# Optimization experiments

Hardware: AMD Instinct MI355X
Metric: run time of the kernel (lower is better)

## Reference

```python
import jax, jax.numpy as jnp
import numpy as np
from jax import lax

H = W = 8
N = H * W            # grid cells
D = 34               # token dim = 16 + 16 + 2
NH = 2               # attention heads
FF = 2048            # torch TransformerEncoderLayer default dim_feedforward
EPS = 1e-5


def setup_inputs():
    key = jax.random.key(0)
    ks = iter(jax.random.split(key, 64))
    rn = lambda shape, s=0.05: jax.random.normal(next(ks), shape, jnp.float32) * s
    inp = {"obs": jax.random.normal(next(ks), (2, H, W), jnp.float32), "action": 2}
    inp["conv1_w"] = rn((16, 2, 3, 3)); inp["conv1_b"] = rn((16,))
    inp["conv2_w"] = rn((16, 16, 3, 3)); inp["conv2_b"] = rn((16,))
    for l in range(2):
        p = f"l{l}_"
        inp[p + "in_w"] = rn((3 * D, D)); inp[p + "in_b"] = rn((3 * D,))
        inp[p + "out_w"] = rn((D, D)); inp[p + "out_b"] = rn((D,))
        inp[p + "ff1_w"] = rn((FF, D)); inp[p + "ff1_b"] = rn((FF,))
        inp[p + "ff2_w"] = rn((D, FF)); inp[p + "ff2_b"] = rn((D,))
        inp[p + "ln1_g"] = jnp.ones((D,)); inp[p + "ln1_b"] = jnp.zeros((D,))
        inp[p + "ln2_g"] = jnp.ones((D,)); inp[p + "ln2_b"] = jnp.zeros((D,))
    inp["act_w"] = rn((8, 4)); inp["act_b"] = rn((8,))
    inp["head_w"] = rn((16, D + 8)); inp["head_b"] = rn((16,))
    return inp


def _ln(x, g, b):
    m = x.mean(-1, keepdims=True)
    v = ((x - m) ** 2).mean(-1, keepdims=True)
    return (x - m) * lax.rsqrt(v + EPS) * g + b


def _mha(x, in_w, in_b, out_w, out_b):
    S = x.shape[0]
    hd = D // NH
    qkv = x @ in_w.T + in_b                          # [S, 3D]
    q, k, v = jnp.split(qkv, 3, axis=-1)
    q = q.reshape(S, NH, hd).transpose(1, 0, 2)      # [H, S, hd]
    k = k.reshape(S, NH, hd).transpose(1, 0, 2)
    v = v.reshape(S, NH, hd).transpose(1, 0, 2)
    attn = jax.nn.softmax(jnp.einsum('hsd,htd->hst', q, k) * (1.0 / float(np.sqrt(hd))), axis=-1)
    o = jnp.einsum('hst,htd->hsd', attn, v).transpose(1, 0, 2).reshape(S, D)
    return o @ out_w.T + out_b


def _layer(x, in_w, in_b, out_w, out_b, ff1_w, ff1_b, ff2_w, ff2_b, ln1_g, ln1_b, ln2_g, ln2_b):
    # torch default post-norm, relu activation, dropout off (eval)
    x = _ln(x + _mha(x, in_w, in_b, out_w, out_b), ln1_g, ln1_b)
    h = jax.nn.relu(x @ ff1_w.T + ff1_b) @ ff2_w.T + ff2_b
    return _ln(x + h, ln2_g, ln2_b)


def _forward(obs, conv1_w, conv1_b, conv2_w, conv2_b, layers, act_w, act_b, head_w, head_b, action):
    x = obs[None]                                    # [1, 2, H, W]
    dn = ('NCHW', 'OIHW', 'NCHW')
    x = jax.nn.relu(lax.conv_general_dilated(x, conv1_w, (1, 1), 'SAME', dimension_numbers=dn) + conv1_b[None, :, None, None])
    x = jax.nn.relu(lax.conv_general_dilated(x, conv2_w, (1, 1), 'SAME', dimension_numbers=dn) + conv2_b[None, :, None, None])
    cell = x.reshape(16, N).T                        # [N, 16]
    # vectorized pairwise relation tokens (replaces O(N^2) python loop)
    r = (jnp.arange(N) // W).astype(jnp.float32)
    c = (jnp.arange(N) % W).astype(jnp.float32)
    dx = (r[:, None] - r[None, :]) / ((H - 1) / 2.0)
    dy = (c[:, None] - c[None, :]) / ((W - 1) / 2.0)
    rel = jnp.stack([dx, dy], axis=-1)               # [N, N, 2]
    a = jnp.broadcast_to(cell[:, None, :], (N, N, 16))
    b = jnp.broadcast_to(cell[None, :, :], (N, N, 16))
    seq = jnp.concatenate([a, b, rel], axis=-1).reshape(N * N, D)
    for p in layers:
        seq = _layer(seq, *p)
    agent_idx = jnp.argmax(obs[0].reshape(-1))
    agent_tok = lax.dynamic_slice_in_dim(seq, agent_idx * N, N, 0)  # rows for agent cell
    hvec = agent_tok.mean(0)
    a_emb = jax.nn.relu(jax.nn.one_hot(action, 4, dtype=jnp.float32) @ act_w.T + act_b)
    return (jnp.concatenate([hvec, a_emb]) @ head_w.T + head_b)[None]


def reference(obs, action, conv1_w, conv1_b, conv2_w, conv2_b,
              l0_in_w, l0_in_b, l0_out_w, l0_out_b, l0_ff1_w, l0_ff1_b, l0_ff2_w, l0_ff2_b,
              l0_ln1_g, l0_ln1_b, l0_ln2_g, l0_ln2_b,
              l1_in_w, l1_in_b, l1_out_w, l1_out_b, l1_ff1_w, l1_ff1_b, l1_ff2_w, l1_ff2_b,
              l1_ln1_g, l1_ln1_b, l1_ln2_g, l1_ln2_b,
              act_w, act_b, head_w, head_b):
    layers = [
        (l0_in_w, l0_in_b, l0_out_w, l0_out_b, l0_ff1_w, l0_ff1_b, l0_ff2_w, l0_ff2_b, l0_ln1_g, l0_ln1_b, l0_ln2_g, l0_ln2_b),
        (l1_in_w, l1_in_b, l1_out_w, l1_out_b, l1_ff1_w, l1_ff1_b, l1_ff2_w, l1_ff2_b, l1_ln1_g, l1_ln1_b, l1_ln2_g, l1_ln2_b),
    ]
    return _forward(obs, conv1_w, conv1_b, conv2_w, conv2_b, layers, act_w, act_b, head_w, head_b, action)
```

## Files before the change

kernel.cpp:

```cpp
#include <hip/hip_runtime.h>
#include <math.h>

#define SEQ 4096
#define DIM 34
#define NHEAD 2
#define HD 17
#define FFDIM 2048
#define SC2 0.34990494f

#define EXP2F(x) __builtin_amdgcn_exp2f(x)
#define MFMA16(a, b, c) __builtin_amdgcn_mfma_f32_16x16x32_bf16(a, b, c, 0, 0, 0)

typedef unsigned short u16;
typedef __attribute__((ext_vector_type(8))) short bf16x8;
typedef __attribute__((ext_vector_type(4))) float f32x4;

__device__ inline u16 f2bf(float f) {
    uint32_t u = __builtin_bit_cast(uint32_t, f);
    u += 0x7fffu + ((u >> 16) & 1u);
    return (u16)(u >> 16);
}
__device__ inline uint32_t pack2(float a, float b) {
    uint32_t ua = __builtin_bit_cast(uint32_t, a);
    ua += 0x7fffu + ((ua >> 16) & 1u);
    uint32_t ub = __builtin_bit_cast(uint32_t, b);
    ub += 0x7fffu + ((ub >> 16) & 1u);
    return (ua >> 16) | (ub & 0xffff0000u);
}

#define W1B_ELEMS (FFDIM * 64)
#define W2B_ELEMS (48 * FFDIM)
#define NWCONV 448

__global__ __launch_bounds__(1024) void wm_pre(
    const float* __restrict__ obs,
    const float* __restrict__ c1w, const float* __restrict__ c1b,
    const float* __restrict__ c2w, const float* __restrict__ c2b,
    const float* __restrict__ in_w, const float* __restrict__ in_b,
    const float* __restrict__ w1a, const float* __restrict__ b1a, const float* __restrict__ w2a,
    const float* __restrict__ w1b, const float* __restrict__ b1b, const float* __restrict__ w2b,
    float* __restrict__ x, u16* __restrict__ Qb, u16* __restrict__ Kb,
    u16* __restrict__ Vc, u16* __restrict__ V16,
    u16* __restrict__ W1A, u16* __restrict__ W2A,
    u16* __restrict__ W1B, u16* __restrict__ W2B)
{
    const int tid = threadIdx.x;
    if (blockIdx.x < NWCONV) {
        int id = blockIdx.x * 1024 + tid;
        const int half = W1B_ELEMS + W2B_ELEMS;
        const float* w1 = w1a; const float* b1 = b1a; const float* w2 = w2a;
        u16* W1 = W1A; u16* W2 = W2A;
        if (id >= half) { id -= half; w1 = w1b; b1 = b1b; w2 = w2b; W1 = W1B; W2 = W2B; }
        if (id < W1B_ELEMS) {
            int n = id >> 6, c = id & 63;
            float v = (c < DIM) ? w1[n*DIM + c] : ((c == DIM) ? b1[n] : 0.f);
            W1[id] = f2bf(v);
        } else {
            int e = id - W1B_ELEMS;
            int n = e >> 11;
            float v = (n < DIM) ? w2[(n << 11) + (e & 2047)] : 0.f;
            W2[e] = f2bf(v);
        }
        return;
    }
    __shared__ float obsp[2][10][10];
    __shared__ float h1p[16][10][10];
    __shared__ float cs[64][17];
    const int sb = blockIdx.x - NWCONV;
    const int t0 = sb * 64;

    for (int e = tid; e < 200; e += 1024) ((float*)obsp)[e] = 0.f;
    for (int e = tid; e < 1600; e += 1024) ((float*)h1p)[e] = 0.f;
    __syncthreads();
    if (tid < 128) {
        int i = tid >> 6, n = tid & 63, y = n >> 3, xx = n & 7;
        obsp[i][y + 1][xx + 1] = obs[tid];
    }
    __syncthreads();
    {
        int o = tid >> 6, n = tid & 63, y = n >> 3, xx = n & 7;
        float a = c1b[o];
        #pragma unroll
        for (int i = 0; i < 2; ++i)
            #pragma unroll
            for (int ky = 0; ky < 3; ++ky)
                #pragma unroll
                for (int kx = 0; kx < 3; ++kx)
                    a = fmaf(obsp[i][y + ky][xx + kx], c1w[((o*2 + i)*3 + ky)*3 + kx], a);
        h1p[o][y + 1][xx + 1] = fmaxf(a, 0.f);
    }
    __syncthreads();
    {
        int o = tid >> 6, n = tid & 63, y = n >> 3, xx = n & 7;
        float a = c2b[o];
        #pragma unroll
        for (int i = 0; i < 16; ++i)
            #pragma unroll
            for (int ky = 0; ky < 3; ++ky)
                #pragma unroll
                for (int kx = 0; kx < 3; ++kx)
                    a = fmaf(h1p[i][y + ky][xx + kx], c2w[((o*16 + i)*3 + ky)*3 + kx], a);
        cs[n][o] = fmaxf(a, 0.f);
    }
    __syncthreads();
    for (int e = tid; e < 64 * DIM; e += 1024) {
        int tl = e / DIM, d = e % DIM;
        int t = t0 + tl, i = t >> 6, j = t & 63;
        float v;
        if (d < 16)       v = cs[i][d];
        else if (d < 32)  v = cs[j][d - 16];
        else if (d == 32) v = (float)((i >> 3) - (j >> 3)) * (1.0f / 3.5f);
        else              v = (float)((i & 7) - (j & 7)) * (1.0f / 3.5f);
        x[t0 * DIM + e] = v;
    }
    for (int ii = 0; ii < 11; ++ii) {
        int e = tid + ii * 1024;
        if (e >= 64 * 162) break;
        int t = t0 + (e & 63), slot = e >> 6;
        int i = t >> 6, j = t & 63;
        float dx = (float)((i >> 3) - (j >> 3)) * (1.0f / 3.5f);
        float dy = (float)((i & 7) - (j & 7)) * (1.0f / 3.5f);
        if (slot < 128) {
            int isK = slot >> 6, h2 = (slot >> 5) & 1, hs = slot & 31;
            float val = 0.f;
            if (hs < HD) {
                int row = isK*DIM + h2*HD + hs;
                const float* wr = in_w + row*DIM;
                float a = in_b[row];
                #pragma unroll
                for (int d = 0; d < 16; ++d) a = fmaf(cs[i][d], wr[d], a);
                #pragma unroll
                for (int d = 0; d < 16; ++d) a = fmaf(cs[j][d], wr[16 + d], a);
                a = fmaf(dx, wr[32], a);
                a = fmaf(dy, wr[33], a);
                val = isK ? a : a * SC2;
            } else if (hs == HD) {
                val = isK ? 1.0f : -8.0f;
            }
            u16* dst = isK ? Kb : Qb;
            dst[(((size_t)h2*SEQ + t) << 5) + hs] = f2bf(val);
        } else {
            int s = slot - 128;
            int h2 = s >= HD, dd = s - h2*HD;
            int row = 2*DIM + h2*HD + dd;
            const float* wr = in_w + row*DIM;
            float a = in_b[row];
            #pragma unroll
            for (int d = 0; d < 16; ++d) a = fmaf(cs[i][d], wr[d], a);
            #pragma unroll
            for (int d = 0; d < 16; ++d) a = fmaf(cs[j][d], wr[16 + d], a);
            a = fmaf(dx, wr[32], a);
            a = fmaf(dy, wr[33], a);
            u16 v = f2bf(a);
            if (dd == 16) V16[h2*SEQ + t] = v;
            else {
                int c = t >> 5, g = (t >> 3) & 3, ix = t & 7;
                Vc[((((size_t)h2*128 + c)*4 + g)*16 + dd)*8 + ix] = v;
            }
        }
    }
}

__global__ __launch_bounds__(1024) void wm_attn3(const u16* __restrict__ Qb,
        const u16* __restrict__ Kb, const u16* __restrict__ Vc,
        const u16* __restrict__ V16, float* __restrict__ x,
        const float* __restrict__ ow, const float* __restrict__ obias,
        const float* __restrict__ g, const float* __restrict__ be)
{
    const int qt = blockIdx.x;
    const int tid = threadIdx.x;
    const int wv = tid >> 6, l = tid & 63;
    const int h = wv >> 3, rr = wv & 7;
    const int q = l & 15, gg = l >> 4;

    __shared__ float red[16][64][7];
    __shared__ float os[16][DIM];
    __shared__ float ys[16][DIM];
    __shared__ float stats[16][2];

    const u16* Qh = Qb + (((size_t)h*SEQ + qt*16 + q) << 5) + 8*gg;
    const u16* Kh = Kb + ((size_t)h*SEQ << 5);
    const u16* Vh = Vc + (size_t)h*128*512;
    const u16* V6 = V16 + (size_t)h*SEQ;

    const bf16x8 qf = *(const bf16x8*)Qh;
    const f32x4 zero4 = {0.f, 0.f, 0.f, 0.f};

    f32x4 olo = zero4, ohi = zero4;
    float ls0 = 0.f, ls1 = 0.f, ls2 = 0.f, ls3 = 0.f;

    const int srcA = q + 32*(gg & 1);
    const int srcB = srcA + 16;
    const bool hi = (gg >= 2);

    for (int it = 0; it < 8; ++it) {
        const int cA = rr*16 + it*2;
        const int k0 = cA * 32;
        bf16x8 kf0 = *(const bf16x8*)(Kh + ((size_t)(k0 + q) << 5) + 8*gg);
        bf16x8 kf1 = *(const bf16x8*)(Kh + ((size_t)(k0 + 16 + q) << 5) + 8*gg);
        bf16x8 kf2 = *(const bf16x8*)(Kh + ((size_t)(k0 + 32 + q) << 5) + 8*gg);
        bf16x8 kf3 = *(const bf16x8*)(Kh + ((size_t)(k0 + 48 + q) << 5) + 8*gg);
        f32x4 s0 = MFMA16(kf0, qf, zero4);
        f32x4 s1 = MFMA16(kf1, qf, zero4);
        f32x4 s2 = MFMA16(kf2, qf, zero4);
        f32x4 s3 = MFMA16(kf3, qf, zero4);
        float pa0 = EXP2F(s0[0]), pa1 = EXP2F(s0[1]), pa2 = EXP2F(s0[2]), pa3 = EXP2F(s0[3]);
        float pa4 = EXP2F(s1[0]), pa5 = EXP2F(s1[1]), pa6 = EXP2F(s1[2]), pa7 = EXP2F(s1[3]);
        float pb0 = EXP2F(s2[0]), pb1 = EXP2F(s2[1]), pb2 = EXP2F(s2[2]), pb3 = EXP2F(s2[3]);
        float pb4 = EXP2F(s3[0]), pb5 = EXP2F(s3[1]), pb6 = EXP2F(s3[2]), pb7 = EXP2F(s3[3]);
        ls0 += (pa0 + pa1) + (pa2 + pa3);
        ls1 += (pa4 + pa5) + (pa6 + pa7);
        ls2 += (pb0 + pb1) + (pb2 + pb3);
        ls3 += (pb4 + pb5) + (pb6 + pb7);
        {
            uint32_t a0t0 = pack2(pa0, pa1), a1t0 = pack2(pa2, pa3);
            uint32_t a0t1 = pack2(pa4, pa5), a1t1 = pack2(pa6, pa7);
            uint32_t w0a = (uint32_t)__shfl((int)a0t0, srcA), w0b = (uint32_t)__shfl((int)a0t1, srcA);
            uint32_t w1a = (uint32_t)__shfl((int)a1t0, srcA), w1b = (uint32_t)__shfl((int)a1t1, srcA);
            uint32_t w2a = (uint32_t)__shfl((int)a0t0, srcB), w2b = (uint32_t)__shfl((int)a0t1, srcB);
            uint32_t w3a = (uint32_t)__shfl((int)a1t0, srcB), w3b = (uint32_t)__shfl((int)a1t1, srcB);
            union { uint32_t u[4]; bf16x8 v; } pu;
            pu.u[0] = hi ? w0b : w0a;
            pu.u[1] = hi ? w1b : w1a;
            pu.u[2] = hi ? w2b : w2a;
            pu.u[3] = hi ? w3b : w3a;
            bf16x8 vf = *(const bf16x8*)(Vh + (size_t)(cA*4 + gg)*128 + q*8);
            bf16x8 v6 = {};
            if (q == 0) v6 = *(const bf16x8*)(V6 + k0 + 8*gg);
            olo = MFMA16(vf, pu.v, olo);
            ohi = MFMA16(v6, pu.v, ohi);
        }
        {
            uint32_t a0t0 = pack2(pb0, pb1), a1t0 = pack2(pb2, pb3);
            uint32_t a0t1 = pack2(pb4, pb5), a1t1 = pack2(pb6, pb7);
            uint32_t w0a = (uint32_t)__shfl((int)a0t0, srcA), w0b = (uint32_t)__shfl((int)a0t1, srcA);
            uint32_t w1a = (uint32_t)__shfl((int)a1t0, srcA), w1b = (uint32_t)__shfl((int)a1t1, srcA);
            uint32_t w2a = (uint32_t)__shfl((int)a0t0, srcB), w2b = (uint32_t)__shfl((int)a0t1, srcB);
            uint32_t w3a = (uint32_t)__shfl((int)a1t0, srcB), w3b = (uint32_t)__shfl((int)a1t1, srcB);
            union { uint32_t u[4]; bf16x8 v; } pu;
            pu.u[0] = hi ? w0b : w0a;
            pu.u[1] = hi ? w1b : w1a;
            pu.u[2] = hi ? w2b : w2a;
            pu.u[3] = hi ? w3b : w3a;
            bf16x8 vf = *(const bf16x8*)(Vh + (size_t)((cA + 1)*4 + gg)*128 + q*8);
            bf16x8 v6 = {};
            if (q == 0) v6 = *(const bf16x8*)(V6 + k0 + 32 + 8*gg);
            olo = MFMA16(vf, pu.v, olo);
            ohi = MFMA16(v6, pu.v, ohi);
        }
    }

    {
        float* r = red[wv][l];
        r[0] = (ls0 + ls1) + (ls2 + ls3);
        r[1] = olo[0]; r[2] = olo[1]; r[3] = olo[2]; r[4] = olo[3];
        r[5] = ohi[0];
    }
    __syncthreads();
    if (rr == 0) {
        float lt = 0.f, o0 = 0.f, o1 = 0.f, o2 = 0.f, o3 = 0.f, o6 = 0.f;
        #pragma unroll
        for (int p = 0; p < 8; ++p) {
            float* r = red[wv + p][l];
            lt += r[0]; o0 += r[1]; o1 += r[2]; o2 += r[3]; o3 += r[4]; o6 += r[5];
        }
        lt += __shfl_xor(lt, 16);
        lt += __shfl_xor(lt, 32);
        float inv = 1.f / lt;
        os[q][h*HD + 4*gg + 0] = o0*inv;
        os[q][h*HD + 4*gg + 1] = o1*inv;
        os[q][h*HD + 4*gg + 2] = o2*inv;
        os[q][h*HD + 4*gg + 3] = o3*inv;
        if (gg == 0) os[q][h*HD + 16] = o6*inv;
    }
    __syncthreads();
    for (int e = tid; e < 16 * DIM; e += 1024) {
        int tt = e / DIM, d = e % DIM;
        const float* wr = ow + d*DIM;
        float acc = obias[d];
        #pragma unroll
        for (int k = 0; k < DIM; ++k) acc = fmaf(os[tt][k], wr[k], acc);
        ys[tt][d] = x[(size_t)(qt*16 + tt)*DIM + d] + acc;
    }
    __syncthreads();
    if (tid < 16) {
        float s1 = 0.f, s2 = 0.f;
        #pragma unroll
        for (int d = 0; d < DIM; ++d) { float v = ys[tid][d]; s1 += v; s2 += v*v; }
        float mean = s1 * (1.0f / DIM);
        float var  = s2 * (1.0f / DIM) - mean*mean;
        stats[tid][0] = mean;
        stats[tid][1] = rsqrtf(var + 1e-5f);
    }
    __syncthreads();
    for (int e = tid; e < 16 * DIM; e += 1024) {
        int tt = e / DIM, d = e % DIM;
        x[(size_t)(qt*16 + tt)*DIM + d] = (ys[tt][d] - stats[tt][0]) * stats[tt][1] * g[d] + be[d];
    }
}

__global__ __launch_bounds__(1024) void wm_ff3(float* __restrict__ x,
        const u16* __restrict__ W1b, const u16* __restrict__ W2b,
        const float* __restrict__ b2, const float* __restrict__ g,
        const float* __restrict__ be,
        const float* __restrict__ in_w, const float* __restrict__ in_b,
        u16* __restrict__ Qb, u16* __restrict__ Kb,
        u16* __restrict__ Vc, u16* __restrict__ V16, int do_qkv)
{
    __shared__ u16 Hs[16][16][128];
    __shared__ float red[16][16][52];
    __shared__ float ys[16][DIM];
    __shared__ float stats[16][2];
    const int tid = threadIdx.x, wv = tid >> 6, l = tid & 63;
    const int q = l & 15, g4 = l >> 4;
    const int t0 = blockIdx.x * 16;

    const float* xr = x + (size_t)(t0 + q) * DIM;
    union { uint32_t u[4]; bf16x8 v; } a0, a1;
    #pragma unroll
    for (int j = 0; j < 4; ++j)
        a0.u[j] = pack2(xr[g4*8 + 2*j], xr[g4*8 + 2*j + 1]);
    a1.u[0] = 0; a1.u[1] = 0; a1.u[2] = 0; a1.u[3] = 0;
    if (g4 == 0) {
        a1.u[0] = pack2(xr[32], xr[33]);
        a1.u[1] = pack2(1.0f, 0.f);
    }
    const f32x4 zero4 = {0.f, 0.f, 0.f, 0.f};

    const int hb = wv * 128;
    #pragma unroll
    for (int nt = 0; nt < 8; ++nt) {
        const u16* brow = W1b + (size_t)(hb + nt*16 + q) * 64 + g4*8;
        bf16x8 b0 = *(const bf16x8*)brow;
        bf16x8 b1f = *(const bf16x8*)(brow + 32);
        f32x4 c = MFMA16(a0.v, b0, zero4);
        c = MFMA16(a1.v, b1f, c);
        #pragma unroll
        for (int r = 0; r < 4; ++r) {
            int mm = 4*g4 + r;
            int byte = ((nt*16 + q) * 2) ^ ((mm & 7) << 4);
            *(u16*)((char*)&Hs[wv][mm][0] + byte) = f2bf(fmaxf(c[r], 0.f));
        }
    }
    asm volatile("s_waitcnt lgkmcnt(0)" ::: "memory");
    __builtin_amdgcn_sched_barrier(0);
    f32x4 acc0 = zero4, acc1 = zero4, acc2 = zero4;
    #pragma unroll
    for (int ks = 0; ks < 4; ++ks) {
        int byte = (ks*64 + g4*16) ^ ((q & 7) << 4);
        bf16x8 af = *(const bf16x8*)((char*)&Hs[wv][q][0] + byte);
        const u16* bp = W2b + (size_t)q * FFDIM + hb + ks*32 + g4*8;
        acc0 = MFMA16(af, *(const bf16x8*)bp, acc0);
        acc1 = MFMA16(af, *(const bf16x8*)(bp + 16*FFDIM), acc1);
        acc2 = MFMA16(af, *(const bf16x8*)(bp + 32*FFDIM), acc2);
    }
    #pragma unroll
    for (int r = 0; r < 4; ++r) {
        red[wv][4*g4 + r][q]      = acc0[r];
        red[wv][4*g4 + r][16 + q] = acc1[r];
        red[wv][4*g4 + r][32 + q] = acc2[r];
    }
    __syncthreads();
    for (int e = tid; e < 16*DIM; e += 1024) {
        int tt = e / DIM, d = e % DIM;
        float v = x[(size_t)(t0 + tt)*DIM + d] + b2[d];
        #pragma unroll
        for (int w = 0; w < 16; ++w) v += red[w][tt][d];
        ys[tt][d] = v;
    }
    __syncthreads();
    if (tid < 16) {
        float s1 = 0.f, s2 = 0.f;
        #pragma unroll
        for (int d = 0; d < DIM; ++d) { float v = ys[tid][d]; s1 += v; s2 += v * v; }
        float mean = s1 * (1.0f / DIM);
        float var  = s2 * (1.0f / DIM) - mean * mean;
        stats[tid][0] = mean;
        stats[tid][1] = rsqrtf(var + 1e-5f);
    }
    __syncthreads();
    for (int e = tid; e < 16*DIM; e += 1024) {
        int tt = e / DIM, d = e % DIM;
        float v = (ys[tt][d] - stats[tt][0]) * stats[tt][1] * g[d] + be[d];
        x[(size_t)(t0 + tt)*DIM + d] = v;
        ys[tt][d] = v;
    }
    if (do_qkv) {
        __syncthreads();
        #pragma unroll
        for (int ii = 0; ii < 2; ++ii) {
            int e = tid + ii*1024;
            if (e < 16*102) {
                int r = e >> 4, tt = e & 15;
                const float* wr = in_w + r*DIM;
                float a = in_b[r];
                #pragma unroll
                for (int d = 0; d < DIM; ++d) a = fmaf(ys[tt][d], wr[d], a);
                int tg = t0 + tt;
                if (r < 68) {
                    int rq = (r < 34) ? r : r - 34;
                    int h2 = rq >= HD, hs = rq - h2*HD;
                    u16 v = f2bf((r < 34) ? a*SC2 : a);
                    u16* dst = (r < 34) ? Qb : Kb;
                    dst[(((size_t)h2*SEQ + tg) << 5) + hs] = v;
                } else {
                    int rv = r - 68;
                    int h2 = rv >= HD, dd = rv - h2*HD;
                    u16 v = f2bf(a);
                    if (dd == 16) V16[h2*SEQ + tg] = v;
                    else {
                        int c = tg >> 5, gg = (tg >> 3) & 3, ix = tg & 7;
                        Vc[((((size_t)h2*128 + c)*4 + gg)*16 + dd)*8 + ix] = v;
                    }
                }
            }
        }
    }
}

__global__ __launch_bounds__(64) void wm_final(const float* __restrict__ x,
        const float* __restrict__ obs, const int* __restrict__ action,
        const float* __restrict__ aw, const float* __restrict__ ab,
        const float* __restrict__ hw, const float* __restrict__ hb,
        float* __restrict__ out)
{
    __shared__ float hv[DIM];
    __shared__ float saemb[8];
    __shared__ int sai;
    const int tid = threadIdx.x;
    {
        float v = obs[tid];
        float mx = v;
        for (int off = 32; off; off >>= 1) mx = fmaxf(mx, __shfl_xor(mx, off));
        unsigned long long mask = __ballot(v == mx);
        if (tid == 0) sai = (int)(__ffsll(mask) - 1);
    }
    if (tid < 8) {
        int act = *action;
        saemb[tid] = fmaxf(aw[tid*4 + act] + ab[tid], 0.f);
    }
    __syncthreads();
    const int ai = sai;
    if (tid < DIM) {
        float s = 0.f;
        for (int r = 0; r < 64; ++r) s += x[(size_t)(ai*64 + r)*DIM + tid];
        hv[tid] = s * (1.0f / 64.0f);
    }
    __syncthreads();
    if (tid < 16) {
        float a = hb[tid];
        #pragma unroll
        for (int d = 0; d < DIM; ++d) a = fmaf(hv[d], hw[tid*42 + d], a);
        #pragma unroll
        for (int j = 0; j < 8; ++j) a = fmaf(saemb[j], hw[tid*42 + DIM + j], a);
        out[tid] = a;
    }
}

extern "C" void kernel_launch(void* const* d_in, const int* in_sizes, int n_in,
                              void* d_out, int out_size, void* d_ws, size_t ws_size,
                              hipStream_t stream)
{
    const float* obs    = (const float*)d_in[0];
    const int*   action = (const int*)  d_in[1];
    const float* c1w = (const float*)d_in[2];
    const float* c1b = (const float*)d_in[3];
    const float* c2w = (const float*)d_in[4];
    const float* c2b = (const float*)d_in[5];
    const float* aw  = (const float*)d_in[30];
    const float* ab  = (const float*)d_in[31];
    const float* hw  = (const float*)d_in[32];
    const float* hb  = (const float*)d_in[33];

    float* ws   = (float*)d_ws;
    float* x    = ws + 1056;
    float* o    = x + SEQ * DIM;
    u16*   Qb   = (u16*)(o + SEQ * DIM);
    u16*   Kb   = Qb + 2 * SEQ * 32;
    u16*   Vc   = Kb + 2 * SEQ * 32;
    u16*   V16  = Vc + 2 * 128 * 512;
    u16*   W1b0 = V16 + 2 * SEQ;
    u16*   W2b0 = W1b0 + W1B_ELEMS;
    u16*   W1b1 = W2b0 + W2B_ELEMS;
    u16*   W2b1 = W1b1 + W1B_ELEMS;

    wm_pre<<<NWCONV + 64, 1024, 0, stream>>>(
        obs, c1w, c1b, c2w, c2b,
        (const float*)d_in[6], (const float*)d_in[7],
        (const float*)d_in[10], (const float*)d_in[11], (const float*)d_in[12],
        (const float*)d_in[22], (const float*)d_in[23], (const float*)d_in[24],
        x, Qb, Kb, Vc, V16, W1b0, W2b0, W1b1, W2b1);

    wm_attn3<<<SEQ / 16, 1024, 0, stream>>>(Qb, Kb, Vc, V16, x,
        (const float*)d_in[8], (const float*)d_in[9],
        (const float*)d_in[14], (const float*)d_in[15]);

    wm_ff3<<<SEQ / 16, 1024, 0, stream>>>(x, W1b0, W2b0,
        (const float*)d_in[13], (const float*)d_in[16], (const float*)d_in[17],
        (const float*)d_in[18], (const float*)d_in[19],
        Qb, Kb, Vc, V16, 1);

    wm_attn3<<<SEQ / 16, 1024, 0, stream>>>(Qb, Kb, Vc, V16, x,
        (const float*)d_in[20], (const float*)d_in[21],
        (const float*)d_in[26], (const float*)d_in[27]);

    wm_ff3<<<SEQ / 16, 1024, 0, stream>>>(x, W1b1, W2b1,
        (const float*)d_in[25], (const float*)d_in[28], (const float*)d_in[29],
        (const float*)d_in[18], (const float*)d_in[19],
        Qb, Kb, Vc, V16, 0);

    wm_final<<<1, 64, 0, stream>>>(x, obs, action, aw, ab, hw, hb, (float*)d_out);
}
```

Measured before the change: 96.70 us.

## Overlap weight conversion with attention, fold final head into FF kernel

```diff
diff --git a/kernel.cpp b/kernel.cpp
--- a/kernel.cpp
+++ b/kernel.cpp
@@ -31,42 +31,22 @@
 #define W1B_ELEMS (FFDIM * 64)
 #define W2B_ELEMS (48 * FFDIM)
 #define NWCONV 448
+#define NQT (SEQ / 16)
 
 __global__ __launch_bounds__(1024) void wm_pre(
     const float* __restrict__ obs,
     const float* __restrict__ c1w, const float* __restrict__ c1b,
     const float* __restrict__ c2w, const float* __restrict__ c2b,
     const float* __restrict__ in_w, const float* __restrict__ in_b,
-    const float* __restrict__ w1a, const float* __restrict__ b1a, const float* __restrict__ w2a,
-    const float* __restrict__ w1b, const float* __restrict__ b1b, const float* __restrict__ w2b,
     float* __restrict__ x, u16* __restrict__ Qb, u16* __restrict__ Kb,
-    u16* __restrict__ Vc, u16* __restrict__ V16,
-    u16* __restrict__ W1A, u16* __restrict__ W2A,
-    u16* __restrict__ W1B, u16* __restrict__ W2B)
+    u16* __restrict__ Vc, u16* __restrict__ V16, int* __restrict__ counter)
 {
     const int tid = threadIdx.x;
-    if (blockIdx.x < NWCONV) {
-        int id = blockIdx.x * 1024 + tid;
-        const int half = W1B_ELEMS + W2B_ELEMS;
-        const float* w1 = w1a; const float* b1 = b1a; const float* w2 = w2a;
-        u16* W1 = W1A; u16* W2 = W2A;
-        if (id >= half) { id -= half; w1 = w1b; b1 = b1b; w2 = w2b; W1 = W1B; W2 = W2B; }
-        if (id < W1B_ELEMS) {
-            int n = id >> 6, c = id & 63;
-            float v = (c < DIM) ? w1[n*DIM + c] : ((c == DIM) ? b1[n] : 0.f);
-            W1[id] = f2bf(v);
-        } else {
-            int e = id - W1B_ELEMS;
-            int n = e >> 11;
-            float v = (n < DIM) ? w2[(n << 11) + (e & 2047)] : 0.f;
-            W2[e] = f2bf(v);
-        }
-        return;
-    }
+    if (blockIdx.x == 0 && tid == 0) *counter = 0;
     __shared__ float obsp[2][10][10];
     __shared__ float h1p[16][10][10];
     __shared__ float cs[64][17];
-    const int sb = blockIdx.x - NWCONV;
+    const int sb = blockIdx.x;
     const int t0 = sb * 64;
 
     for (int e = tid; e < 200; e += 1024) ((float*)obsp)[e] = 0.f;
@@ -165,10 +145,32 @@
         const u16* __restrict__ Kb, const u16* __restrict__ Vc,
         const u16* __restrict__ V16, float* __restrict__ x,
         const float* __restrict__ ow, const float* __restrict__ obias,
-        const float* __restrict__ g, const float* __restrict__ be)
+        const float* __restrict__ g, const float* __restrict__ be,
+        const float* __restrict__ w1a, const float* __restrict__ b1a, const float* __restrict__ w2a,
+        const float* __restrict__ w1b, const float* __restrict__ b1b, const float* __restrict__ w2b,
+        u16* __restrict__ W1A, u16* __restrict__ W2A,
+        u16* __restrict__ W1B, u16* __restrict__ W2B)
 {
     const int qt = blockIdx.x;
     const int tid = threadIdx.x;
+    if (qt >= NQT) {
+        int id = (qt - NQT) * 1024 + tid;
+        const int half = W1B_ELEMS + W2B_ELEMS;
+        const float* w1 = w1a; const float* b1 = b1a; const float* w2 = w2a;
+        u16* W1 = W1A; u16* W2 = W2A;
+        if (id >= half) { id -= half; w1 = w1b; b1 = b1b; w2 = w2b; W1 = W1B; W2 = W2B; }
+        if (id < W1B_ELEMS) {
+            int n = id >> 6, c = id & 63;
+            float v = (c < DIM) ? w1[n*DIM + c] : ((c == DIM) ? b1[n] : 0.f);
+            W1[id] = f2bf(v);
+        } else {
+            int e = id - W1B_ELEMS;
+            int n = e >> 11;
+            float v = (n < DIM) ? w2[(n << 11) + (e & 2047)] : 0.f;
+            W2[e] = f2bf(v);
+        }
+        return;
+    }
     const int wv = tid >> 6, l = tid & 63;
     const int h = wv >> 3, rr = wv & 7;
     const int q = l & 15, gg = l >> 4;
@@ -185,10 +187,11 @@
 
     const bf16x8 qf = *(const bf16x8*)Qh;
     const f32x4 zero4 = {0.f, 0.f, 0.f, 0.f};
+    bf16x8 onesv;
+    { union { uint32_t u[4]; bf16x8 v; } o1;
+      o1.u[0] = o1.u[1] = o1.u[2] = o1.u[3] = 0x3F803F80u; onesv = o1.v; }
 
     f32x4 olo = zero4, ohi = zero4;
-    float ls0 = 0.f, ls1 = 0.f, ls2 = 0.f, ls3 = 0.f;
-
     const int srcA = q + 32*(gg & 1);
     const int srcB = srcA + 16;
     const bool hi = (gg >= 2);
@@ -208,25 +211,22 @@
         float pa4 = EXP2F(s1[0]), pa5 = EXP2F(s1[1]), pa6 = EXP2F(s1[2]), pa7 = EXP2F(s1[3]);
         float pb0 = EXP2F(s2[0]), pb1 = EXP2F(s2[1]), pb2 = EXP2F(s2[2]), pb3 = EXP2F(s2[3]);
         float pb4 = EXP2F(s3[0]), pb5 = EXP2F(s3[1]), pb6 = EXP2F(s3[2]), pb7 = EXP2F(s3[3]);
-        ls0 += (pa0 + pa1) + (pa2 + pa3);
-        ls1 += (pa4 + pa5) + (pa6 + pa7);
-        ls2 += (pb0 + pb1) + (pb2 + pb3);
-        ls3 += (pb4 + pb5) + (pb6 + pb7);
         {
             uint32_t a0t0 = pack2(pa0, pa1), a1t0 = pack2(pa2, pa3);
             uint32_t a0t1 = pack2(pa4, pa5), a1t1 = pack2(pa6, pa7);
             uint32_t w0a = (uint32_t)__shfl((int)a0t0, srcA), w0b = (uint32_t)__shfl((int)a0t1, srcA);
-            uint32_t w1a = (uint32_t)__shfl((int)a1t0, srcA), w1b = (uint32_t)__shfl((int)a1t1, srcA);
-            uint32_t w2a = (uint32_t)__shfl((int)a0t0, srcB), w2b = (uint32_t)__shfl((int)a0t1, srcB);
+            uint32_t w1a_ = (uint32_t)__shfl((int)a1t0, srcA), w1b_ = (uint32_t)__shfl((int)a1t1, srcA);
+            uint32_t w2a_ = (uint32_t)__shfl((int)a0t0, srcB), w2b_ = (uint32_t)__shfl((int)a0t1, srcB);
             uint32_t w3a = (uint32_t)__shfl((int)a1t0, srcB), w3b = (uint32_t)__shfl((int)a1t1, srcB);
             union { uint32_t u[4]; bf16x8 v; } pu;
             pu.u[0] = hi ? w0b : w0a;
-            pu.u[1] = hi ? w1b : w1a;
-            pu.u[2] = hi ? w2b : w2a;
+            pu.u[1] = hi ? w1b_ : w1a_;
+            pu.u[2] = hi ? w2b_ : w2a_;
             pu.u[3] = hi ? w3b : w3a;
             bf16x8 vf = *(const bf16x8*)(Vh + (size_t)(cA*4 + gg)*128 + q*8);
             bf16x8 v6 = {};
             if (q == 0) v6 = *(const bf16x8*)(V6 + k0 + 8*gg);
+            else if (q == 1) v6 = onesv;
             olo = MFMA16(vf, pu.v, olo);
             ohi = MFMA16(v6, pu.v, ohi);
         }
@@ -234,17 +234,18 @@
             uint32_t a0t0 = pack2(pb0, pb1), a1t0 = pack2(pb2, pb3);
             uint32_t a0t1 = pack2(pb4, pb5), a1t1 = pack2(pb6, pb7);
             uint32_t w0a = (uint32_t)__shfl((int)a0t0, srcA), w0b = (uint32_t)__shfl((int)a0t1, srcA);
-            uint32_t w1a = (uint32_t)__shfl((int)a1t0, srcA), w1b = (uint32_t)__shfl((int)a1t1, srcA);
-            uint32_t w2a = (uint32_t)__shfl((int)a0t0, srcB), w2b = (uint32_t)__shfl((int)a0t1, srcB);
+            uint32_t w1a_ = (uint32_t)__shfl((int)a1t0, srcA), w1b_ = (uint32_t)__shfl((int)a1t1, srcA);
+            uint32_t w2a_ = (uint32_t)__shfl((int)a0t0, srcB), w2b_ = (uint32_t)__shfl((int)a0t1, srcB);
             uint32_t w3a = (uint32_t)__shfl((int)a1t0, srcB), w3b = (uint32_t)__shfl((int)a1t1, srcB);
             union { uint32_t u[4]; bf16x8 v; } pu;
             pu.u[0] = hi ? w0b : w0a;
-            pu.u[1] = hi ? w1b : w1a;
-            pu.u[2] = hi ? w2b : w2a;
+            pu.u[1] = hi ? w1b_ : w1a_;
+            pu.u[2] = hi ? w2b_ : w2a_;
             pu.u[3] = hi ? w3b : w3a;
             bf16x8 vf = *(const bf16x8*)(Vh + (size_t)((cA + 1)*4 + gg)*128 + q*8);
             bf16x8 v6 = {};
             if (q == 0) v6 = *(const bf16x8*)(V6 + k0 + 32 + 8*gg);
+            else if (q == 1) v6 = onesv;
             olo = MFMA16(vf, pu.v, olo);
             ohi = MFMA16(v6, pu.v, ohi);
         }
@@ -252,7 +253,7 @@
 
     {
         float* r = red[wv][l];
-        r[0] = (ls0 + ls1) + (ls2 + ls3);
+        r[0] = ohi[1];
         r[1] = olo[0]; r[2] = olo[1]; r[3] = olo[2]; r[4] = olo[3];
         r[5] = ohi[0];
     }
@@ -305,7 +306,11 @@
         const float* __restrict__ be,
         const float* __restrict__ in_w, const float* __restrict__ in_b,
         u16* __restrict__ Qb, u16* __restrict__ Kb,
-        u16* __restrict__ Vc, u16* __restrict__ V16, int do_qkv)
+        u16* __restrict__ Vc, u16* __restrict__ V16, int do_qkv, int do_final,
+        const float* __restrict__ obs, const int* __restrict__ action,
+        const float* __restrict__ aw, const float* __restrict__ ab,
+        const float* __restrict__ hw, const float* __restrict__ hb,
+        float* __restrict__ out, int* __restrict__ counter)
 {
     __shared__ u16 Hs[16][16][128];
     __shared__ float red[16][16][52];
@@ -327,10 +332,10 @@
     }
     const f32x4 zero4 = {0.f, 0.f, 0.f, 0.f};
 
-    const int hb = wv * 128;
+    const int hbase = wv * 128;
     #pragma unroll
     for (int nt = 0; nt < 8; ++nt) {
-        const u16* brow = W1b + (size_t)(hb + nt*16 + q) * 64 + g4*8;
+        const u16* brow = W1b + (size_t)(hbase + nt*16 + q) * 64 + g4*8;
         bf16x8 b0 = *(const bf16x8*)brow;
         bf16x8 b1f = *(const bf16x8*)(brow + 32);
         f32x4 c = MFMA16(a0.v, b0, zero4);
@@ -349,7 +354,7 @@
     for (int ks = 0; ks < 4; ++ks) {
         int byte = (ks*64 + g4*16) ^ ((q & 7) << 4);
         bf16x8 af = *(const bf16x8*)((char*)&Hs[wv][q][0] + byte);
-        const u16* bp = W2b + (size_t)q * FFDIM + hb + ks*32 + g4*8;
+        const u16* bp = W2b + (size_t)q * FFDIM + hbase + ks*32 + g4*8;
         acc0 = MFMA16(af, *(const bf16x8*)bp, acc0);
         acc1 = MFMA16(af, *(const bf16x8*)(bp + 16*FFDIM), acc1);
         acc2 = MFMA16(af, *(const bf16x8*)(bp + 32*FFDIM), acc2);
@@ -416,44 +421,46 @@
             }
         }
     }
-}
-
-__global__ __launch_bounds__(64) void wm_final(const float* __restrict__ x,
-        const float* __restrict__ obs, const int* __restrict__ action,
-        const float* __restrict__ aw, const float* __restrict__ ab,
-        const float* __restrict__ hw, const float* __restrict__ hb,
-        float* __restrict__ out)
-{
-    __shared__ float hv[DIM];
-    __shared__ float saemb[8];
-    __shared__ int sai;
-    const int tid = threadIdx.x;
-    {
-        float v = obs[tid];
-        float mx = v;
-        for (int off = 32; off; off >>= 1) mx = fmaxf(mx, __shfl_xor(mx, off));
-        unsigned long long mask = __ballot(v == mx);
-        if (tid == 0) sai = (int)(__ffsll(mask) - 1);
-    }
-    if (tid < 8) {
-        int act = *action;
-        saemb[tid] = fmaxf(aw[tid*4 + act] + ab[tid], 0.f);
-    }
-    __syncthreads();
-    const int ai = sai;
-    if (tid < DIM) {
-        float s = 0.f;
-        for (int r = 0; r < 64; ++r) s += x[(size_t)(ai*64 + r)*DIM + tid];
-        hv[tid] = s * (1.0f / 64.0f);
-    }
-    __syncthreads();
-    if (tid < 16) {
-        float a = hb[tid];
-        #pragma unroll
-        for (int d = 0; d < DIM; ++d) a = fmaf(hv[d], hw[tid*42 + d], a);
-        #pragma unroll
-        for (int j = 0; j < 8; ++j) a = fmaf(saemb[j], hw[tid*42 + DIM + j], a);
-        out[tid] = a;
+
+    if (do_final) {
+        __shared__ int slast;
+        __shared__ float hv[DIM];
+        __shared__ float saemb[8];
+        __shared__ int sai;
+        __threadfence();
+        __syncthreads();
+        if (tid == 0) slast = (atomicAdd(counter, 1) == (int)gridDim.x - 1) ? 1 : 0;
+        __syncthreads();
+        if (!slast) return;
+        __threadfence();
+        if (tid < 64) {
+            float v = obs[tid];
+            float mx = v;
+            for (int off = 32; off; off >>= 1) mx = fmaxf(mx, __shfl_xor(mx, off));
+            unsigned long long mask = __ballot(v == mx);
+            if (tid == 0) sai = (int)(__ffsll(mask) - 1);
+        }
+        if (tid >= 64 && tid < 72) {
+            int k = tid - 64;
+            int act = *action;
+            saemb[k] = fmaxf(aw[k*4 + act] + ab[k], 0.f);
+        }
+        __syncthreads();
+        const int ai = sai;
+        if (tid < DIM) {
+            float sacc = 0.f;
+            for (int r = 0; r < 64; ++r) sacc += x[(size_t)(ai*64 + r)*DIM + tid];
+            hv[tid] = sacc * (1.0f / 64.0f);
+        }
+        __syncthreads();
+        if (tid < 16) {
+            float a = hb[tid];
+            #pragma unroll
+            for (int d = 0; d < DIM; ++d) a = fmaf(hv[d], hw[tid*42 + d], a);
+            #pragma unroll
+            for (int j = 0; j < 8; ++j) a = fmaf(saemb[j], hw[tid*42 + DIM + j], a);
+            out[tid] = a;
+        }
     }
 }
 
@@ -463,16 +470,9 @@
 {
     const float* obs    = (const float*)d_in[0];
     const int*   action = (const int*)  d_in[1];
-    const float* c1w = (const float*)d_in[2];
-    const float* c1b = (const float*)d_in[3];
-    const float* c2w = (const float*)d_in[4];
-    const float* c2b = (const float*)d_in[5];
-    const float* aw  = (const float*)d_in[30];
-    const float* ab  = (const float*)d_in[31];
-    const float* hw  = (const float*)d_in[32];
-    const float* hb  = (const float*)d_in[33];
 
     float* ws   = (float*)d_ws;
+    int*   cnt  = (int*)ws;
     float* x    = ws + 1056;
     float* o    = x + SEQ * DIM;
     u16*   Qb   = (u16*)(o + SEQ * DIM);
@@ -484,30 +484,37 @@
     u16*   W1b1 = W2b0 + W2B_ELEMS;
     u16*   W2b1 = W1b1 + W1B_ELEMS;
 
-    wm_pre<<<NWCONV + 64, 1024, 0, stream>>>(
-        obs, c1w, c1b, c2w, c2b,
+    wm_pre<<<64, 1024, 0, stream>>>(
+        obs, (const float*)d_in[2], (const float*)d_in[3],
+        (const float*)d_in[4], (const float*)d_in[5],
         (const float*)d_in[6], (const float*)d_in[7],
+        x, Qb, Kb, Vc, V16, cnt);
+
+    wm_attn3<<<NQT + NWCONV, 1024, 0, stream>>>(Qb, Kb, Vc, V16, x,
+        (const float*)d_in[8], (const float*)d_in[9],
+        (const float*)d_in[14], (const float*)d_in[15],
         (const float*)d_in[10], (const float*)d_in[11], (const float*)d_in[12],
         (const float*)d_in[22], (const float*)d_in[23], (const float*)d_in[24],
-        x, Qb, Kb, Vc, V16, W1b0, W2b0, W1b1, W2b1);
-
-    wm_attn3<<<SEQ / 16, 1024, 0, stream>>>(Qb, Kb, Vc, V16, x,
-        (const float*)d_in[8], (const float*)d_in[9],
-        (const float*)d_in[14], (const float*)d_in[15]);
-
-    wm_ff3<<<SEQ / 16, 1024, 0, stream>>>(x, W1b0, W2b0,
+        W1b0, W2b0, W1b1, W2b1);
+
+    wm_ff3<<<NQT, 1024, 0, stream>>>(x, W1b0, W2b0,
         (const float*)d_in[13], (const float*)d_in[16], (const float*)d_in[17],
         (const float*)d_in[18], (const float*)d_in[19],
-        Qb, Kb, Vc, V16, 1);
-
-    wm_attn3<<<SEQ / 16, 1024, 0, stream>>>(Qb, Kb, Vc, V16, x,
+        Qb, Kb, Vc, V16, 1, 0,
+        obs, action, (const float*)d_in[30], (const float*)d_in[31],
+        (const float*)d_in[32], (const float*)d_in[33], (float*)d_out, cnt);
+
+    wm_attn3<<<NQT, 1024, 0, stream>>>(Qb, Kb, Vc, V16, x,
         (const float*)d_in[20], (const float*)d_in[21],
-        (const float*)d_in[26], (const float*)d_in[27]);
-
-    wm_ff3<<<SEQ / 16, 1024, 0, stream>>>(x, W1b1, W2b1,
+        (const float*)d_in[26], (const float*)d_in[27],
+        (const float*)d_in[10], (const float*)d_in[11], (const float*)d_in[12],
+        (const float*)d_in[22], (const float*)d_in[23], (const float*)d_in[24],
+        W1b0, W2b0, W1b1, W2b1);
+
+    wm_ff3<<<NQT, 1024, 0, stream>>>(x, W1b1, W2b1,
         (const float*)d_in[25], (const float*)d_in[28], (const float*)d_in[29],
         (const float*)d_in[18], (const float*)d_in[19],
-        Qb, Kb, Vc, V16, 0);
-
-    wm_final<<<1, 64, 0, stream>>>(x, obs, action, aw, ab, hw, hb, (float*)d_out);
+        Qb, Kb, Vc, V16, 0, 1,
+        obs, action, (const float*)d_in[30], (const float*)d_in[31],
+        (const float*)d_in[32], (const float*)d_in[33], (float*)d_out, cnt);
 }
```

Measured after the change: 159.7 us. 1.65x slower.
